# Kernel tuning notes

Hardware: AMD Instinct MI355X
Metric: run time of the kernel (lower is better)

The kernel has to match this reference:

```python
import jax, jax.numpy as jnp
import numpy as np

N_CELLS, D_IN, D_HID, D_OUT, MLP_W = 16384, 512, 1024, 512, 128
N_FACTIONS, SYNC, DEBATE = 8, 0.15, 0.15


def setup_inputs() -> dict:
    key = jax.random.key(0)
    ks = jax.random.split(key, 20)
    s = 0.05
    inp = {
        "x": jax.random.normal(ks[0], (1, D_IN), jnp.float32),
        "hiddens": jax.random.normal(ks[1], (N_CELLS, D_HID), jnp.float32) * 0.1,
        "wealth_norm": jax.random.uniform(ks[2], (N_CELLS,), jnp.float32, 0.5, 1.5),
        "Wa1": jax.random.normal(ks[3], (D_IN + D_HID, MLP_W), jnp.float32) * s,
        "ba1": jax.random.normal(ks[4], (MLP_W,), jnp.float32) * s,
        "Wa2": jax.random.normal(ks[5], (MLP_W, D_OUT), jnp.float32) * s,
        "ba2": jax.random.normal(ks[6], (D_OUT,), jnp.float32) * s,
        "Wg1": jax.random.normal(ks[7], (D_IN + D_HID, MLP_W), jnp.float32) * s,
        "bg1": jax.random.normal(ks[8], (MLP_W,), jnp.float32) * s,
        "Wg2": jax.random.normal(ks[9], (MLP_W, D_OUT), jnp.float32) * s,
        "bg2": jax.random.normal(ks[10], (D_OUT,), jnp.float32) * s,
        "W_ih": jax.random.normal(ks[11], (D_OUT + 1, 3 * D_HID), jnp.float32) * s,
        "W_hh": jax.random.normal(ks[12], (D_HID, 3 * D_HID), jnp.float32) * s,
        "b_ih": jax.random.normal(ks[13], (3 * D_HID,), jnp.float32) * s,
        "b_hh": jax.random.normal(ks[14], (3 * D_HID,), jnp.float32) * s,
        "Wo": jax.random.normal(ks[15], (D_OUT, D_IN), jnp.float32) * s,
        "bo": jax.random.normal(ks[16], (D_IN,), jnp.float32) * s,
        "positions": jax.random.randint(ks[17], (N_CELLS,), 0, 3, jnp.int32) - 1,
        "step": 10,
    }
    return inp


def _gru_cell(mem, h, W_ih, W_hh, b_ih, b_hh):
    # torch.nn.GRUCell math, gate order r, z, n
    gi = mem @ W_ih + b_ih            # [N, 3H]
    gh = h @ W_hh + b_hh              # [N, 3H]
    gi_r, gi_z, gi_n = jnp.split(gi, 3, axis=-1)
    gh_r, gh_z, gh_n = jnp.split(gh, 3, axis=-1)
    r = jax.nn.sigmoid(gi_r + gh_r)
    z = jax.nn.sigmoid(gi_z + gh_z)
    n = jnp.tanh(gi_n + r * gh_n)
    return (1.0 - z) * n + z * h


def _group_sync(h, mask):
    cnt = jnp.sum(mask)
    m = mask[:, None].astype(h.dtype)
    mean = jnp.sum(h * m, axis=0) / jnp.maximum(cnt, 1).astype(h.dtype)
    blended = 0.9 * h + 0.1 * mean
    return jnp.where((mask[:, None]) & (cnt >= 2), blended, h)


def _faction_sync_debate(h, step):
    n = h.shape[0]
    n_f = min(N_FACTIONS, n // 2)
    if n_f < 2:
        return h
    fs = n // n_f
    hf = h[: n_f * fs].reshape(n_f, fs, -1)
    fmean = hf.mean(axis=1, keepdims=True)                    # [n_f, 1, H]
    hf = (1.0 - SYNC) * hf + SYNC * fmean
    if step > 5:
        global_op = hf.mean(axis=1).mean(axis=0)              # [H]
        dc = max(1, fs // 4)
        head = (1.0 - DEBATE) * hf[:, :dc] + DEBATE * global_op
        hf = jnp.concatenate([head, hf[:, dc:]], axis=1)
    out = hf.reshape(n_f * fs, -1)
    if n_f * fs < n:
        out = jnp.concatenate([out, h[n_f * fs:]], axis=0)
    return out


def reference(x, hiddens, wealth_norm, Wa1, ba1, Wa2, ba2, Wg1, bg1, Wg2, bg2,
              W_ih, W_hh, b_ih, b_hh, Wo, bo, positions, step):
    n = hiddens.shape[0]
    xb = jnp.broadcast_to(x, (n, x.shape[-1]))                # same x for every cell
    combined = jnp.concatenate([xb, hiddens], axis=-1)        # [N, D_in+D_hid]
    a = jax.nn.relu(combined @ Wa1 + ba1) @ Wa2 + ba2
    g = jax.nn.relu(combined @ Wg1 + bg1) @ Wg2 + bg2
    output = a - g                                            # [N, D_out]
    tension = jnp.mean(output ** 2, axis=-1, keepdims=True)   # [N, 1]
    mem_input = jax.lax.stop_gradient(jnp.concatenate([output, tension], axis=-1))
    new_h = _gru_cell(mem_input, hiddens, W_ih, W_hh, b_ih, b_hh)
    mod = 0.9 + 0.1 * jnp.clip(wealth_norm, 0.1, 2.0)
    new_h = jnp.clip(new_h * mod[:, None], -10.0, 10.0)
    new_h = jax.lax.stop_gradient(new_h)                      # original detaches state
    new_h = _group_sync(new_h, positions > 0)
    new_h = _group_sync(new_h, positions < 0)
    new_h = _faction_sync_debate(new_h, step)
    # tension weights come from .item() in torch -> constants
    weights = jax.nn.softmax(jax.lax.stop_gradient(tension[:, 0]))
    combined_out = weights @ output                           # [D_out]
    pred = (combined_out @ Wo + bo)[None, :]                  # [1, D_in]
    avg_tension = jnp.mean(tension)
    return pred, avg_tension, new_h
```

## Files before the change

### kernel.cpp

```cpp
#include <hip/hip_runtime.h>
#include <stdint.h>

typedef unsigned short u16;
typedef __bf16 bf16x8 __attribute__((ext_vector_type(8)));
typedef float f32x4 __attribute__((ext_vector_type(4)));


__device__ __forceinline__ float bf2f(unsigned u) { return __uint_as_float(u << 16); }
__device__ __forceinline__ u16 f2bf(float f) {
  unsigned x = __float_as_uint(f);
  unsigned r = x + 0x7fffu + ((x >> 16) & 1u);
  return (u16)(r >> 16);
}
__device__ __forceinline__ void unpack8(uint4 v, float* o) {
  o[0] = bf2f(v.x & 0xffff); o[1] = bf2f(v.x >> 16);
  o[2] = bf2f(v.y & 0xffff); o[3] = bf2f(v.y >> 16);
  o[4] = bf2f(v.z & 0xffff); o[5] = bf2f(v.z >> 16);
  o[6] = bf2f(v.w & 0xffff); o[7] = bf2f(v.w >> 16);
}
__device__ __forceinline__ float sigm(float x) { return 1.f / (1.f + __expf(-x)); }

#define AS1(p) ((const __attribute__((address_space(1))) void*)(p))
#define AS3(p) ((__attribute__((address_space(3))) void*)(p))

#define NC 16384

__global__ void cvt_hid_kernel(const float4* __restrict__ src, uint4* __restrict__ dst) {
  int i = blockIdx.x * 256 + threadIdx.x;
  float4 a = src[(size_t)i * 2], b = src[(size_t)i * 2 + 1];
  union { u16 o[8]; uint4 v; } u;
  u.o[0] = f2bf(a.x); u.o[1] = f2bf(a.y); u.o[2] = f2bf(a.z); u.o[3] = f2bf(a.w);
  u.o[4] = f2bf(b.x); u.o[5] = f2bf(b.y); u.o[6] = f2bf(b.z); u.o[7] = f2bf(b.w);
  dst[i] = u.v;
}

__global__ __launch_bounds__(256) void packT_kernel(
    const float* __restrict__ src, int sld, int srow0,
    u16* __restrict__ dst, int dld, int drow0, int koff,
    int remapThresh, int remapAdd, float sgn) {
  __shared__ float tile[64][65];
  const int k0 = blockIdx.y * 64, c0 = blockIdx.x * 64;
  const int t = threadIdx.x;
  const int tx = t & 15, ty = t >> 4;
#pragma unroll
  for (int p = 0; p < 4; ++p) {
    int r = ty + p * 16;
    float4 v = *reinterpret_cast<const float4*>(&src[(size_t)(srow0 + k0 + r) * sld + c0 + tx * 4]);
    tile[tx * 4 + 0][r] = v.x;
    tile[tx * 4 + 1][r] = v.y;
    tile[tx * 4 + 2][r] = v.z;
    tile[tx * 4 + 3][r] = v.w;
  }
  __syncthreads();
  const int cl = t >> 2;
  const int kb = (t & 3) * 16;
  int col = c0 + cl;
  int row = drow0 + col + ((col >= remapThresh) ? remapAdd : 0);
  union { u16 o[16]; uint4 v[2]; } u;
#pragma unroll
  for (int e = 0; e < 16; ++e) u.o[e] = f2bf(sgn * tile[cl][kb + e]);
  uint4* d = reinterpret_cast<uint4*>(&dst[(size_t)row * dld + koff + k0 + kb]);
  d[0] = u.v[0]; d[1] = u.v[1];
}

__global__ void bias1_kernel(const float* __restrict__ x, const float* __restrict__ Wa1f,
                             const float* __restrict__ ba1f, const float* __restrict__ Wg1f,
                             const float* __restrict__ bg1f, float* __restrict__ bias1) {
  int c = threadIdx.x;
  const float* W = (c < 128) ? Wa1f : Wg1f;
  int cc = c & 127;
  float acc = 0.f;
  int k0 = blockIdx.x * 64;
  for (int k = k0; k < k0 + 64; ++k) acc += x[k] * W[(size_t)k * 128 + cc];
  if (blockIdx.x == 0) acc += (c < 128) ? ba1f[cc] : bg1f[cc];
  atomicAdd(&bias1[c], acc);
}
__global__ void bias2_kernel(const float* __restrict__ ba2f, const float* __restrict__ bg2f,
                             float* __restrict__ bias2) {
  int n = blockIdx.x * 256 + threadIdx.x;
  bias2[n] = ba2f[n] - bg2f[n];
}

__global__ __launch_bounds__(256) void gemm_bt(
    const u16* __restrict__ A0, int lda0, int kbound,
    const u16* __restrict__ A1, int lda1,
    const u16* __restrict__ Bt, int ldb,
    u16* __restrict__ C, int ldc,
    const float* __restrict__ bias, int epi, int Ktot, int gru) {
  __shared__ __align__(16) u16 As[128 * 32];
  __shared__ __align__(16) u16 Bs[128 * 32];
  const int tid = threadIdx.x;
  const int m0 = blockIdx.x * 128;
  const int n0 = blockIdx.y * 128;
  int kbeg = 0, kend = Ktot;
  if (gru) {
    int region = n0 >> 10;
    if (region == 2) kend = 512;
    if (region == 3) kbeg = 512;
  }
  f32x4 acc[4][4] = {};
  const int lane = tid & 63;
  const int w = tid >> 6;
  const int mw = (w & 1) * 64, nw = (w >> 1) * 64;
  const int fr = lane & 15;
  const int kq = (lane >> 4) * 8;
  const int c0 = tid, c1 = tid + 256;
  const int ar0 = c0 >> 2, ak0 = (c0 & 3) * 8;
  const int ar1 = c1 >> 2, ak1 = (c1 & 3) * 8;

  for (int kk = kbeg; kk < kend; kk += 32) {
    const u16* Aseg; int lda, ko;
    if (kk < kbound) { Aseg = A0; lda = lda0; ko = kk; }
    else             { Aseg = A1; lda = lda1; ko = kk - kbound; }
    __syncthreads();
    __builtin_amdgcn_global_load_lds(AS1(Aseg + (size_t)(m0 + ar0) * lda + ko + ak0), AS3(&As[c0 * 8]), 16, 0, 0);
    __builtin_amdgcn_global_load_lds(AS1(Aseg + (size_t)(m0 + ar1) * lda + ko + ak1), AS3(&As[c1 * 8]), 16, 0, 0);
    __builtin_amdgcn_global_load_lds(AS1(Bt + (size_t)(n0 + ar0) * ldb + kk + ak0), AS3(&Bs[c0 * 8]), 16, 0, 0);
    __builtin_amdgcn_global_load_lds(AS1(Bt + (size_t)(n0 + ar1) * ldb + kk + ak1), AS3(&Bs[c1 * 8]), 16, 0, 0);
    __syncthreads();
    bf16x8 af[4], bfv[4];
#pragma unroll
    for (int mt = 0; mt < 4; ++mt)
      af[mt] = *reinterpret_cast<const bf16x8*>(&As[(mw + mt * 16 + fr) * 32 + kq]);
#pragma unroll
    for (int nt = 0; nt < 4; ++nt)
      bfv[nt] = *reinterpret_cast<const bf16x8*>(&Bs[(nw + nt * 16 + fr) * 32 + kq]);
#pragma unroll
    for (int mt = 0; mt < 4; ++mt)
#pragma unroll
      for (int nt = 0; nt < 4; ++nt)
        acc[mt][nt] = __builtin_amdgcn_mfma_f32_16x16x32_bf16(af[mt], bfv[nt], acc[mt][nt], 0, 0, 0);
  }
  const int rq = (lane >> 4) * 4;
#pragma unroll
  for (int mt = 0; mt < 4; ++mt) {
#pragma unroll
    for (int nt = 0; nt < 4; ++nt) {
      int col = n0 + nw + nt * 16 + (lane & 15);
      f32x4 v = acc[mt][nt];
#pragma unroll
      for (int r = 0; r < 4; ++r) {
        int row = m0 + mw + mt * 16 + rq + r;
        float val = v[r];
        if (epi == 1) { val += bias[col]; val = val > 0.f ? val : 0.f; }
        else if (epi == 2) { val += bias[col]; }
        C[(size_t)row * ldc + col] = f2bf(val);
      }
    }
  }
}

__global__ void tension_kernel(const u16* __restrict__ outbf, float* __restrict__ tension) {
  int w = threadIdx.x >> 6, lane = threadIdx.x & 63;
  int row = blockIdx.x * 4 + w;
  uint4 v = *reinterpret_cast<const uint4*>(outbf + (size_t)row * 512 + lane * 8);
  float o[8]; unpack8(v, o);
  float s = 0.f;
#pragma unroll
  for (int e = 0; e < 8; ++e) s += o[e] * o[e];
  for (int off = 32; off; off >>= 1) s += __shfl_down(s, off, 64);
  if (lane == 0) tension[row] = s * (1.f / 512.f);
}

__global__ void gate_kernel(const u16* __restrict__ pre, const u16* __restrict__ hidc,
                            const float* __restrict__ W_ihf, const float* __restrict__ bihf,
                            const float* __restrict__ bhhf, const float* __restrict__ wealthf,
                            const float* __restrict__ tension, u16* __restrict__ hpre,
                            int rowStart) {
  int rl = blockIdx.x, row = rowStart + rl, t = threadIdx.x, j = t * 8;
  const u16* prow = pre + (size_t)rl * 4096;
  const float* wihtf = W_ihf + (size_t)512 * 3072;
  float tv = tension[row];
  float wl = fminf(fmaxf(wealthf[row], 0.1f), 2.0f);
  float mod = 0.9f + 0.1f * wl;
  float pr[8], pz[8], pn1[8], pn2[8], hv[8];
  float wtr[8], wtz[8], wtn[8], bir[8], biz[8], bin_[8], bhn[8], bhr4[8], bhz4[8];
  unpack8(*reinterpret_cast<const uint4*>(prow + j), pr);
  unpack8(*reinterpret_cast<const uint4*>(prow + 1024 + j), pz);
  unpack8(*reinterpret_cast<const uint4*>(prow + 2048 + j), pn1);
  unpack8(*reinterpret_cast<const uint4*>(prow + 3072 + j), pn2);
  unpack8(*reinterpret_cast<const uint4*>(hidc + (size_t)row * 1024 + j), hv);
#pragma unroll
  for (int q = 0; q < 2; ++q) {
    *reinterpret_cast<float4*>(&wtr[q * 4]) = *reinterpret_cast<const float4*>(wihtf + j + q * 4);
    *reinterpret_cast<float4*>(&wtz[q * 4]) = *reinterpret_cast<const float4*>(wihtf + 1024 + j + q * 4);
    *reinterpret_cast<float4*>(&wtn[q * 4]) = *reinterpret_cast<const float4*>(wihtf + 2048 + j + q * 4);
    *reinterpret_cast<float4*>(&bir[q * 4]) = *reinterpret_cast<const float4*>(bihf + j + q * 4);
    *reinterpret_cast<float4*>(&biz[q * 4]) = *reinterpret_cast<const float4*>(bihf + 1024 + j + q * 4);
    *reinterpret_cast<float4*>(&bin_[q * 4]) = *reinterpret_cast<const float4*>(bihf + 2048 + j + q * 4);
    *reinterpret_cast<float4*>(&bhr4[q * 4]) = *reinterpret_cast<const float4*>(bhhf + j + q * 4);
    *reinterpret_cast<float4*>(&bhz4[q * 4]) = *reinterpret_cast<const float4*>(bhhf + 1024 + j + q * 4);
    *reinterpret_cast<float4*>(&bhn[q * 4]) = *reinterpret_cast<const float4*>(bhhf + 2048 + j + q * 4);
  }
  union { u16 o[8]; uint4 v; } u;
#pragma unroll
  for (int e = 0; e < 8; ++e) {
    float r = sigm(pr[e] + tv * wtr[e] + bir[e] + bhr4[e]);
    float z = sigm(pz[e] + tv * wtz[e] + biz[e] + bhz4[e]);
    float n = tanhf(pn1[e] + tv * wtn[e] + bin_[e] + r * (pn2[e] + bhn[e]));
    float h2 = (1.f - z) * n + z * hv[e];
    h2 = fminf(fmaxf(h2 * mod, -10.f), 10.f);
    u.o[e] = f2bf(h2);
  }
  *reinterpret_cast<uint4*>(hpre + (size_t)row * 1024 + j) = u.v;
}

__global__ void count_kernel(const int* __restrict__ positions, int* __restrict__ counts) {
  int i = blockIdx.x * 256 + threadIdx.x;
  if (i < NC) {
    int p = positions[i], f = i >> 11;
    if (p > 0) atomicAdd(&counts[f * 2], 1);
    else if (p < 0) atomicAdd(&counts[f * 2 + 1], 1);
  }
}

__global__ void stats_kernel(const u16* __restrict__ hpre, const int* __restrict__ positions,
                             float* __restrict__ fsums) {
  int cc = blockIdx.x, f = blockIdx.y, z = blockIdx.z, t = threadIdx.x;
  int col = cc * 128 + (t & 127);
  int half = t >> 7;
  float st = 0, sp = 0, sm = 0;
  for (int it = 0; it < 128; ++it) {
    int row = (f << 11) + ((z * 128 + it) << 1) + half;
    int p = positions[row];
    float v = bf2f(hpre[(size_t)row * 1024 + col]);
    st += v;
    if (p > 0) sp += v;
    if (p < 0) sm += v;
  }
  atomicAdd(&fsums[(f * 3 + 0) * 1024 + col], st);
  atomicAdd(&fsums[(f * 3 + 1) * 1024 + col], sp);
  atomicAdd(&fsums[(f * 3 + 2) * 1024 + col], sm);
}

__global__ void derive_kernel(const float* __restrict__ fsums, const int* __restrict__ counts,
                              float* __restrict__ mean1, float* __restrict__ mean2,
                              float* __restrict__ fmean, float* __restrict__ gop,
                              float* __restrict__ scal) {
  int c = threadIdx.x;
  int cnt1 = 0, cnt2 = 0, cf1[8], cf2[8];
#pragma unroll
  for (int f = 0; f < 8; ++f) {
    cf1[f] = counts[f * 2]; cf2[f] = counts[f * 2 + 1];
    cnt1 += cf1[f]; cnt2 += cf2[f];
  }
  float s1 = 0, s2 = 0;
#pragma unroll
  for (int f = 0; f < 8; ++f) { s1 += fsums[(f * 3 + 1) * 1024 + c]; s2 += fsums[(f * 3 + 2) * 1024 + c]; }
  float m1 = s1 / (float)(cnt1 > 1 ? cnt1 : 1);
  float m2 = s2 / (float)(cnt2 > 1 ? cnt2 : 1);
  float a1 = (cnt1 >= 2) ? 0.1f : 0.f;
  float a2 = (cnt2 >= 2) ? 0.1f : 0.f;
  float g = 0;
#pragma unroll
  for (int f = 0; f < 8; ++f) {
    float fm = (fsums[(f * 3) * 1024 + c]
                + a1 * ((float)cf1[f] * m1 - fsums[(f * 3 + 1) * 1024 + c])
                + a2 * ((float)cf2[f] * m2 - fsums[(f * 3 + 2) * 1024 + c])) * (1.f / 2048.f);
    fmean[f * 1024 + c] = fm;
    g += fm;
  }
  gop[c] = g * 0.125f;
  mean1[c] = m1; mean2[c] = m2;
  if (c == 0) { scal[0] = a1; scal[1] = a2; }
}

__global__ void finalize_kernel(const u16* __restrict__ hpre, const int* __restrict__ positions,
                                const int* __restrict__ step, const float* __restrict__ mean1,
                                const float* __restrict__ mean2, const float* __restrict__ fmean,
                                const float* __restrict__ gop, const float* __restrict__ scal,
                                float* __restrict__ out) {
  int row = blockIdx.x, t = threadIdx.x;
  int p = positions[row];
  float w1 = (p > 0) ? scal[0] : 0.f;
  float w2 = (p < 0) ? scal[1] : 0.f;
  int f = row >> 11, q = row & 2047;
  bool deb = (step[0] > 5) && (q < 512);
  const u16* hrow = hpre + (size_t)row * 1024;
  const float* fmp = fmean + f * 1024;
  float* orow = out + 513 + (size_t)row * 1024;
#pragma unroll
  for (int e = 0; e < 8; ++e) {
    int c = e * 128 + t;
    float h = bf2f(hrow[c]);
    float hgs = h + w1 * (mean1[c] - h) + w2 * (mean2[c] - h);
    float hfs = 0.85f * hgs + 0.15f * fmp[c];
    orow[c] = deb ? (0.85f * hfs + 0.15f * gop[c]) : hfs;
  }
}

__global__ void softmax_kernel(const float* __restrict__ tension, float* __restrict__ weights,
                               float* __restrict__ out) {
  __shared__ float red[1024];
  int t = threadIdx.x;
  float tv[16], mx = -1e30f, sumt = 0.f;
#pragma unroll
  for (int k = 0; k < 16; ++k) {
    tv[k] = tension[t + k * 1024];
    mx = fmaxf(mx, tv[k]); sumt += tv[k];
  }
  red[t] = mx; __syncthreads();
  for (int s = 512; s > 0; s >>= 1) { if (t < s) red[t] = fmaxf(red[t], red[t + s]); __syncthreads(); }
  float m = red[0]; __syncthreads();
  red[t] = sumt; __syncthreads();
  for (int s = 512; s > 0; s >>= 1) { if (t < s) red[t] += red[t + s]; __syncthreads(); }
  float tot = red[0]; __syncthreads();
  float ev[16], se = 0.f;
#pragma unroll
  for (int k = 0; k < 16; ++k) { ev[k] = __expf(tv[k] - m); se += ev[k]; }
  red[t] = se; __syncthreads();
  for (int s = 512; s > 0; s >>= 1) { if (t < s) red[t] += red[t + s]; __syncthreads(); }
  float invS = 1.f / red[0];
#pragma unroll
  for (int k = 0; k < 16; ++k) weights[t + k * 1024] = ev[k] * invS;
  if (t == 0) out[512] = tot * (1.f / 16384.f);
}

__global__ void wsum_kernel(const float* __restrict__ weights, const u16* __restrict__ outbf,
                            float* __restrict__ co) {
  int b = blockIdx.x, t = threadIdx.x;
  int c = t * 2;
  float a0 = 0.f, a1 = 0.f;
  int i0 = b * 128;
  for (int i = i0; i < i0 + 128; ++i) {
    float w = weights[i];
    unsigned v = *reinterpret_cast<const unsigned*>(outbf + (size_t)i * 512 + c);
    a0 += w * bf2f(v & 0xffff);
    a1 += w * bf2f(v >> 16);
  }
  atomicAdd(&co[c], a0);
  atomicAdd(&co[c + 1], a1);
}

__global__ void pred_kernel(const float* __restrict__ co, const float* __restrict__ Wof,
                            const float* __restrict__ bof, float* __restrict__ out) {
  __shared__ float cs[512];
  int t = threadIdx.x, n = blockIdx.x * 256 + t;
  cs[t] = co[t]; cs[t + 256] = co[t + 256];
  __syncthreads();
  float acc = bof[n];
  for (int ck = 0; ck < 512; ++ck) acc += cs[ck] * Wof[(size_t)ck * 512 + n];
  out[n] = acc;
}

extern "C" void kernel_launch(void* const* d_in, const int* in_sizes, int n_in,
                              void* d_out, int out_size, void* d_ws, size_t ws_size,
                              hipStream_t stream) {
  const float* x      = (const float*)d_in[0];
  const float* hid    = (const float*)d_in[1];
  const float* wealth = (const float*)d_in[2];
  const float* Wa1    = (const float*)d_in[3];
  const float* ba1    = (const float*)d_in[4];
  const float* Wa2    = (const float*)d_in[5];
  const float* ba2    = (const float*)d_in[6];
  const float* Wg1    = (const float*)d_in[7];
  const float* bg1    = (const float*)d_in[8];
  const float* Wg2    = (const float*)d_in[9];
  const float* bg2    = (const float*)d_in[10];
  const float* W_ih   = (const float*)d_in[11];
  const float* W_hh   = (const float*)d_in[12];
  const float* b_ih   = (const float*)d_in[13];
  const float* b_hh   = (const float*)d_in[14];
  const float* Wo     = (const float*)d_in[15];
  const float* bo     = (const float*)d_in[16];
  const int* positions= (const int*)d_in[17];
  const int* step     = (const int*)d_in[18];
  float* out = (float*)d_out;

  char* w = (char*)d_ws;
  size_t off = 0;
  auto alloc = [&](size_t bytes) { void* p = w + off; off += (bytes + 255) & ~(size_t)255; return p; };
  u16*   hidc    = (u16*)  alloc((size_t)NC * 1024 * 2);
  u16*   outbf   = (u16*)  alloc((size_t)NC * 512 * 2);
  u16*   hpre    = (u16*)  alloc((size_t)NC * 1024 * 2);
  u16*   WgruT   = (u16*)  alloc((size_t)4096 * 1536 * 2);
  u16*   W1catT  = (u16*)  alloc((size_t)256 * 1024 * 2);
  u16*   W2catT  = (u16*)  alloc((size_t)512 * 256 * 2);
  float* bias1   = (float*)alloc(256 * 4);
  float* co      = (float*)alloc(512 * 4);
  int*   counts  = (int*)  alloc(16 * 4);
  float* fsums   = (float*)alloc(8 * 3 * 1024 * 4);
  float* bias2   = (float*)alloc(512 * 4);
  float* tension = (float*)alloc(NC * 4);
  float* weights = (float*)alloc(NC * 4);
  float* mean1   = (float*)alloc(1024 * 4);
  float* mean2   = (float*)alloc(1024 * 4);
  float* gop     = (float*)alloc(1024 * 4);
  float* fmean   = (float*)alloc(8 * 1024 * 4);
  float* scal    = (float*)alloc(8 * 4);
  size_t fixed = off;
  size_t t1Bytes = (size_t)NC * 256 * 2;
  size_t avail = ws_size > fixed ? ws_size - fixed : 0;
  int R = 16384;
  while (R > 1024 && (size_t)R * 4096 * 2 > avail) R >>= 1;
  size_t uBytes = (size_t)R * 4096 * 2; if (uBytes < t1Bytes) uBytes = t1Bytes;
  u16* t1 = (u16*)alloc(uBytes);
  u16* preact = t1;
  int nch = NC / R;

  hipMemsetAsync(bias1, 0, 1024 + 2048 + 256 + 98304, stream);

  cvt_hid_kernel<<<8192, 256, 0, stream>>>((const float4*)hid, (uint4*)hidc);
  packT_kernel<<<dim3(2, 16), 256, 0, stream>>>(Wa1, 128, 512, W1catT, 1024, 0, 0, 1 << 30, 0, 1.f);
  packT_kernel<<<dim3(2, 16), 256, 0, stream>>>(Wg1, 128, 512, W1catT, 1024, 128, 0, 1 << 30, 0, 1.f);
  packT_kernel<<<dim3(8, 2), 256, 0, stream>>>(Wa2, 512, 0, W2catT, 256, 0, 0, 1 << 30, 0, 1.f);
  packT_kernel<<<dim3(8, 2), 256, 0, stream>>>(Wg2, 512, 0, W2catT, 256, 0, 128, 1 << 30, 0, -1.f);
  packT_kernel<<<dim3(48, 8), 256, 0, stream>>>(W_ih, 3072, 0, WgruT, 1536, 0, 0, 1 << 30, 0, 1.f);
  packT_kernel<<<dim3(48, 16), 256, 0, stream>>>(W_hh, 3072, 0, WgruT, 1536, 0, 512, 2048, 1024, 1.f);
  bias1_kernel<<<8, 256, 0, stream>>>(x, Wa1, ba1, Wg1, bg1, bias1);
  bias2_kernel<<<2, 256, 0, stream>>>(ba2, bg2, bias2);
  count_kernel<<<64, 256, 0, stream>>>(positions, counts);

  gemm_bt<<<dim3(128, 2), 256, 0, stream>>>(hidc, 1024, 1024, hidc, 1024,
                                            W1catT, 1024, t1, 256, bias1, 1, 1024, 0);
  gemm_bt<<<dim3(128, 4), 256, 0, stream>>>(t1, 256, 256, t1, 256,
                                            W2catT, 256, outbf, 512, bias2, 2, 256, 0);
  tension_kernel<<<4096, 256, 0, stream>>>(outbf, tension);

  for (int c = 0; c < nch; ++c) {
    const u16* A0 = outbf + (size_t)c * R * 512;
    const u16* A1 = hidc + (size_t)c * R * 1024;
    gemm_bt<<<dim3(R / 128, 32), 256, 0, stream>>>(A0, 512, 512, A1, 1024,
                                                   WgruT, 1536, preact, 4096, nullptr, 0, 1536, 1);
    gate_kernel<<<R, 128, 0, stream>>>(preact, hidc, W_ih, b_ih, b_hh, wealth,
                                       tension, hpre, c * R);
  }

  stats_kernel<<<dim3(8, 8, 8), 256, 0, stream>>>(hpre, positions, fsums);
  derive_kernel<<<1, 1024, 0, stream>>>(fsums, counts, mean1, mean2, fmean, gop, scal);
  finalize_kernel<<<NC, 128, 0, stream>>>(hpre, positions, step, mean1, mean2, fmean, gop,
                                          scal, out);

  softmax_kernel<<<1, 1024, 0, stream>>>(tension, weights, out);
  wsum_kernel<<<128, 256, 0, stream>>>(weights, outbf, co);
  pred_kernel<<<2, 256, 0, stream>>>(co, Wo, bo, out);

  (void)in_sizes; (void)n_in; (void)out_size;
}
```

Measured before the change: 685.3 us.

## Fuse GRU gate math into GEMM epilogue and merge prep/small kernels

Replaces the GRU preactivation GEMM plus a separate gate kernel with one gemm_gru kernel. Each block computes the r, z, n_input and n_hidden tiles for a 64-column slice and applies the gate nonlinearity in registers, so the 16384x4096 bf16 preactivation buffer is never written to or read back from global memory. The tension reduction is folded into the second MLP GEMM's epilogue through shuffles and atomics. The conversion, packing and small bias/count kernels are merged into two launches. The risks are atomic float accumulation order, a fast tanh approximation, and the register pressure of four accumulator sets per block.

```diff
diff --git a/kernel.cpp b/kernel.cpp
--- a/kernel.cpp
+++ b/kernel.cpp
@@ -12,35 +12,23 @@
   unsigned r = x + 0x7fffu + ((x >> 16) & 1u);
   return (u16)(r >> 16);
 }
-__device__ __forceinline__ void unpack8(uint4 v, float* o) {
-  o[0] = bf2f(v.x & 0xffff); o[1] = bf2f(v.x >> 16);
-  o[2] = bf2f(v.y & 0xffff); o[3] = bf2f(v.y >> 16);
-  o[4] = bf2f(v.z & 0xffff); o[5] = bf2f(v.z >> 16);
-  o[6] = bf2f(v.w & 0xffff); o[7] = bf2f(v.w >> 16);
-}
 __device__ __forceinline__ float sigm(float x) { return 1.f / (1.f + __expf(-x)); }
+__device__ __forceinline__ float fast_tanh(float x) {
+  float e = __expf(2.f * x);
+  return 1.f - 2.f / (e + 1.f);
+}
 
 #define AS1(p) ((const __attribute__((address_space(1))) void*)(p))
 #define AS3(p) ((__attribute__((address_space(3))) void*)(p))
 
 #define NC 16384
 
-__global__ void cvt_hid_kernel(const float4* __restrict__ src, uint4* __restrict__ dst) {
-  int i = blockIdx.x * 256 + threadIdx.x;
-  float4 a = src[(size_t)i * 2], b = src[(size_t)i * 2 + 1];
-  union { u16 o[8]; uint4 v; } u;
-  u.o[0] = f2bf(a.x); u.o[1] = f2bf(a.y); u.o[2] = f2bf(a.z); u.o[3] = f2bf(a.w);
-  u.o[4] = f2bf(b.x); u.o[5] = f2bf(b.y); u.o[6] = f2bf(b.z); u.o[7] = f2bf(b.w);
-  dst[i] = u.v;
-}
-
-__global__ __launch_bounds__(256) void packT_kernel(
+__device__ __forceinline__ void packT_body(
     const float* __restrict__ src, int sld, int srow0,
     u16* __restrict__ dst, int dld, int drow0, int koff,
-    int remapThresh, int remapAdd, float sgn) {
-  __shared__ float tile[64][65];
-  const int k0 = blockIdx.y * 64, c0 = blockIdx.x * 64;
-  const int t = threadIdx.x;
+    int remapThresh, int remapAdd, float sgn, int bx, int by,
+    float (*tile)[65], int t) {
+  const int k0 = by * 64, c0 = bx * 64;
   const int tx = t & 15, ty = t >> 4;
 #pragma unroll
   for (int p = 0; p < 4; ++p) {
@@ -63,60 +51,104 @@
   d[0] = u.v[0]; d[1] = u.v[1];
 }
 
-__global__ void bias1_kernel(const float* __restrict__ x, const float* __restrict__ Wa1f,
-                             const float* __restrict__ ba1f, const float* __restrict__ Wg1f,
-                             const float* __restrict__ bg1f, float* __restrict__ bias1) {
-  int c = threadIdx.x;
-  const float* W = (c < 128) ? Wa1f : Wg1f;
-  int cc = c & 127;
-  float acc = 0.f;
-  int k0 = blockIdx.x * 64;
-  for (int k = k0; k < k0 + 64; ++k) acc += x[k] * W[(size_t)k * 128 + cc];
-  if (blockIdx.x == 0) acc += (c < 128) ? ba1f[cc] : bg1f[cc];
-  atomicAdd(&bias1[c], acc);
-}
-__global__ void bias2_kernel(const float* __restrict__ ba2f, const float* __restrict__ bg2f,
-                             float* __restrict__ bias2) {
-  int n = blockIdx.x * 256 + threadIdx.x;
-  bias2[n] = ba2f[n] - bg2f[n];
+__global__ __launch_bounds__(256) void prep_kernel(
+    const float* __restrict__ hid, u16* __restrict__ hidc,
+    const float* __restrict__ W_ih, const float* __restrict__ W_hh, u16* __restrict__ WgruT,
+    const float* __restrict__ Wa1, const float* __restrict__ Wg1, u16* __restrict__ W1catT,
+    const float* __restrict__ Wa2, const float* __restrict__ Wg2, u16* __restrict__ W2catT) {
+  __shared__ float tile[64][65];
+  int b = blockIdx.x, t = threadIdx.x;
+  if (b < 8192) {
+    int i = b * 256 + t;
+    const float4* s = (const float4*)hid;
+    float4 a = s[(size_t)i * 2], c = s[(size_t)i * 2 + 1];
+    union { u16 o[8]; uint4 v; } u;
+    u.o[0] = f2bf(a.x); u.o[1] = f2bf(a.y); u.o[2] = f2bf(a.z); u.o[3] = f2bf(a.w);
+    u.o[4] = f2bf(c.x); u.o[5] = f2bf(c.y); u.o[6] = f2bf(c.z); u.o[7] = f2bf(c.w);
+    ((uint4*)hidc)[i] = u.v;
+    return;
+  }
+  b -= 8192;
+  if (b < 768) {
+    packT_body(W_hh, 3072, 0, WgruT, 1536, 0, 512, 2048, 1024, 1.f, b % 48, b / 48, tile, t);
+    return;
+  }
+  b -= 768;
+  if (b < 384) {
+    packT_body(W_ih, 3072, 0, WgruT, 1536, 0, 0, 1 << 30, 0, 1.f, b % 48, b / 48, tile, t);
+    return;
+  }
+  b -= 384;
+  if (b < 32) {
+    packT_body(Wa1, 128, 512, W1catT, 1024, 0, 0, 1 << 30, 0, 1.f, b % 2, b / 2, tile, t);
+    return;
+  }
+  b -= 32;
+  if (b < 32) {
+    packT_body(Wg1, 128, 512, W1catT, 1024, 128, 0, 1 << 30, 0, 1.f, b % 2, b / 2, tile, t);
+    return;
+  }
+  b -= 32;
+  if (b < 16) {
+    packT_body(Wa2, 512, 0, W2catT, 256, 0, 0, 1 << 30, 0, 1.f, b % 8, b / 8, tile, t);
+    return;
+  }
+  b -= 16;
+  packT_body(Wg2, 512, 0, W2catT, 256, 0, 128, 1 << 30, 0, -1.f, b % 8, b / 8, tile, t);
+}
+
+__global__ void smalls_kernel(const float* __restrict__ x, const float* __restrict__ Wa1,
+                              const float* __restrict__ ba1, const float* __restrict__ Wg1,
+                              const float* __restrict__ bg1, float* __restrict__ bias1,
+                              const float* __restrict__ ba2, const float* __restrict__ bg2,
+                              float* __restrict__ bias2, const int* __restrict__ positions,
+                              int* __restrict__ counts) {
+  int b = blockIdx.x, t = threadIdx.x;
+  if (b < 8) {
+    const float* W = (t < 128) ? Wa1 : Wg1;
+    int cc = t & 127;
+    float acc = 0.f;
+    int k0 = b * 64;
+    for (int k = k0; k < k0 + 64; ++k) acc += x[k] * W[(size_t)k * 128 + cc];
+    if (b == 0) acc += (t < 128) ? ba1[cc] : bg1[cc];
+    atomicAdd(&bias1[t], acc);
+  } else if (b < 10) {
+    int n = (b - 8) * 256 + t;
+    bias2[n] = ba2[n] - bg2[n];
+  } else {
+    int i = (b - 10) * 256 + t;
+    int p = positions[i], f = i >> 11;
+    if (p > 0) atomicAdd(&counts[f * 2], 1);
+    else if (p < 0) atomicAdd(&counts[f * 2 + 1], 1);
+  }
 }
 
 __global__ __launch_bounds__(256) void gemm_bt(
-    const u16* __restrict__ A0, int lda0, int kbound,
-    const u16* __restrict__ A1, int lda1,
+    const u16* __restrict__ A, int lda,
     const u16* __restrict__ Bt, int ldb,
     u16* __restrict__ C, int ldc,
-    const float* __restrict__ bias, int epi, int Ktot, int gru) {
+    const float* __restrict__ bias, int epi, int K,
+    float* __restrict__ tension) {
   __shared__ __align__(16) u16 As[128 * 32];
   __shared__ __align__(16) u16 Bs[128 * 32];
   const int tid = threadIdx.x;
   const int m0 = blockIdx.x * 128;
   const int n0 = blockIdx.y * 128;
-  int kbeg = 0, kend = Ktot;
-  if (gru) {
-    int region = n0 >> 10;
-    if (region == 2) kend = 512;
-    if (region == 3) kbeg = 512;
-  }
   f32x4 acc[4][4] = {};
   const int lane = tid & 63;
   const int w = tid >> 6;
   const int mw = (w & 1) * 64, nw = (w >> 1) * 64;
   const int fr = lane & 15;
   const int kq = (lane >> 4) * 8;
-  const int c0 = tid, c1 = tid + 256;
-  const int ar0 = c0 >> 2, ak0 = (c0 & 3) * 8;
-  const int ar1 = c1 >> 2, ak1 = (c1 & 3) * 8;
-
-  for (int kk = kbeg; kk < kend; kk += 32) {
-    const u16* Aseg; int lda, ko;
-    if (kk < kbound) { Aseg = A0; lda = lda0; ko = kk; }
-    else             { Aseg = A1; lda = lda1; ko = kk - kbound; }
+  const int ar0 = tid >> 2, ak0 = (tid & 3) * 8;
+  const int ar1 = ar0 + 64;
+
+  for (int kk = 0; kk < K; kk += 32) {
     __syncthreads();
-    __builtin_amdgcn_global_load_lds(AS1(Aseg + (size_t)(m0 + ar0) * lda + ko + ak0), AS3(&As[c0 * 8]), 16, 0, 0);
-    __builtin_amdgcn_global_load_lds(AS1(Aseg + (size_t)(m0 + ar1) * lda + ko + ak1), AS3(&As[c1 * 8]), 16, 0, 0);
-    __builtin_amdgcn_global_load_lds(AS1(Bt + (size_t)(n0 + ar0) * ldb + kk + ak0), AS3(&Bs[c0 * 8]), 16, 0, 0);
-    __builtin_amdgcn_global_load_lds(AS1(Bt + (size_t)(n0 + ar1) * ldb + kk + ak1), AS3(&Bs[c1 * 8]), 16, 0, 0);
+    __builtin_amdgcn_global_load_lds(AS1(A + (size_t)(m0 + ar0) * lda + kk + ak0), AS3(&As[tid * 8]), 16, 0, 0);
+    __builtin_amdgcn_global_load_lds(AS1(A + (size_t)(m0 + ar1) * lda + kk + ak0), AS3(&As[(tid + 256) * 8]), 16, 0, 0);
+    __builtin_amdgcn_global_load_lds(AS1(Bt + (size_t)(n0 + ar0) * ldb + kk + ak0), AS3(&Bs[tid * 8]), 16, 0, 0);
+    __builtin_amdgcn_global_load_lds(AS1(Bt + (size_t)(n0 + ar1) * ldb + kk + ak0), AS3(&Bs[(tid + 256) * 8]), 16, 0, 0);
     __syncthreads();
     bf16x8 af[4], bfv[4];
 #pragma unroll
@@ -134,83 +166,130 @@
   const int rq = (lane >> 4) * 4;
 #pragma unroll
   for (int mt = 0; mt < 4; ++mt) {
+    float srow[4] = {0.f, 0.f, 0.f, 0.f};
 #pragma unroll
     for (int nt = 0; nt < 4; ++nt) {
-      int col = n0 + nw + nt * 16 + (lane & 15);
+      int col = n0 + nw + nt * 16 + fr;
       f32x4 v = acc[mt][nt];
 #pragma unroll
       for (int r = 0; r < 4; ++r) {
         int row = m0 + mw + mt * 16 + rq + r;
-        float val = v[r];
-        if (epi == 1) { val += bias[col]; val = val > 0.f ? val : 0.f; }
-        else if (epi == 2) { val += bias[col]; }
+        float val = v[r] + bias[col];
+        if (epi == 1) val = val > 0.f ? val : 0.f;
+        else srow[r] += val * val;
         C[(size_t)row * ldc + col] = f2bf(val);
       }
     }
-  }
-}
-
-__global__ void tension_kernel(const u16* __restrict__ outbf, float* __restrict__ tension) {
-  int w = threadIdx.x >> 6, lane = threadIdx.x & 63;
-  int row = blockIdx.x * 4 + w;
-  uint4 v = *reinterpret_cast<const uint4*>(outbf + (size_t)row * 512 + lane * 8);
-  float o[8]; unpack8(v, o);
-  float s = 0.f;
-#pragma unroll
-  for (int e = 0; e < 8; ++e) s += o[e] * o[e];
-  for (int off = 32; off; off >>= 1) s += __shfl_down(s, off, 64);
-  if (lane == 0) tension[row] = s * (1.f / 512.f);
-}
-
-__global__ void gate_kernel(const u16* __restrict__ pre, const u16* __restrict__ hidc,
-                            const float* __restrict__ W_ihf, const float* __restrict__ bihf,
-                            const float* __restrict__ bhhf, const float* __restrict__ wealthf,
-                            const float* __restrict__ tension, u16* __restrict__ hpre,
-                            int rowStart) {
-  int rl = blockIdx.x, row = rowStart + rl, t = threadIdx.x, j = t * 8;
-  const u16* prow = pre + (size_t)rl * 4096;
-  const float* wihtf = W_ihf + (size_t)512 * 3072;
-  float tv = tension[row];
-  float wl = fminf(fmaxf(wealthf[row], 0.1f), 2.0f);
-  float mod = 0.9f + 0.1f * wl;
-  float pr[8], pz[8], pn1[8], pn2[8], hv[8];
-  float wtr[8], wtz[8], wtn[8], bir[8], biz[8], bin_[8], bhn[8], bhr4[8], bhz4[8];
-  unpack8(*reinterpret_cast<const uint4*>(prow + j), pr);
-  unpack8(*reinterpret_cast<const uint4*>(prow + 1024 + j), pz);
-  unpack8(*reinterpret_cast<const uint4*>(prow + 2048 + j), pn1);
-  unpack8(*reinterpret_cast<const uint4*>(prow + 3072 + j), pn2);
-  unpack8(*reinterpret_cast<const uint4*>(hidc + (size_t)row * 1024 + j), hv);
-#pragma unroll
-  for (int q = 0; q < 2; ++q) {
-    *reinterpret_cast<float4*>(&wtr[q * 4]) = *reinterpret_cast<const float4*>(wihtf + j + q * 4);
-    *reinterpret_cast<float4*>(&wtz[q * 4]) = *reinterpret_cast<const float4*>(wihtf + 1024 + j + q * 4);
-    *reinterpret_cast<float4*>(&wtn[q * 4]) = *reinterpret_cast<const float4*>(wihtf + 2048 + j + q * 4);
-    *reinterpret_cast<float4*>(&bir[q * 4]) = *reinterpret_cast<const float4*>(bihf + j + q * 4);
-    *reinterpret_cast<float4*>(&biz[q * 4]) = *reinterpret_cast<const float4*>(bihf + 1024 + j + q * 4);
-    *reinterpret_cast<float4*>(&bin_[q * 4]) = *reinterpret_cast<const float4*>(bihf + 2048 + j + q * 4);
-    *reinterpret_cast<float4*>(&bhr4[q * 4]) = *reinterpret_cast<const float4*>(bhhf + j + q * 4);
-    *reinterpret_cast<float4*>(&bhz4[q * 4]) = *reinterpret_cast<const float4*>(bhhf + 1024 + j + q * 4);
-    *reinterpret_cast<float4*>(&bhn[q * 4]) = *reinterpret_cast<const float4*>(bhhf + 2048 + j + q * 4);
-  }
-  union { u16 o[8]; uint4 v; } u;
-#pragma unroll
-  for (int e = 0; e < 8; ++e) {
-    float r = sigm(pr[e] + tv * wtr[e] + bir[e] + bhr4[e]);
-    float z = sigm(pz[e] + tv * wtz[e] + biz[e] + bhz4[e]);
-    float n = tanhf(pn1[e] + tv * wtn[e] + bin_[e] + r * (pn2[e] + bhn[e]));
-    float h2 = (1.f - z) * n + z * hv[e];
-    h2 = fminf(fmaxf(h2 * mod, -10.f), 10.f);
-    u.o[e] = f2bf(h2);
-  }
-  *reinterpret_cast<uint4*>(hpre + (size_t)row * 1024 + j) = u.v;
-}
-
-__global__ void count_kernel(const int* __restrict__ positions, int* __restrict__ counts) {
-  int i = blockIdx.x * 256 + threadIdx.x;
-  if (i < NC) {
-    int p = positions[i], f = i >> 11;
-    if (p > 0) atomicAdd(&counts[f * 2], 1);
-    else if (p < 0) atomicAdd(&counts[f * 2 + 1], 1);
+    if (epi == 3) {
+#pragma unroll
+      for (int r = 0; r < 4; ++r) {
+        float s = srow[r];
+        s += __shfl_xor(s, 1, 16); s += __shfl_xor(s, 2, 16);
+        s += __shfl_xor(s, 4, 16); s += __shfl_xor(s, 8, 16);
+        if (fr == 0) atomicAdd(&tension[m0 + mw + mt * 16 + rq + r], s);
+      }
+    }
+  }
+}
+
+__global__ __launch_bounds__(256, 2) void gemm_gru(
+    const u16* __restrict__ outbf, const u16* __restrict__ hidc,
+    const u16* __restrict__ WgruT,
+    const float* __restrict__ W_ihf, const float* __restrict__ bihf,
+    const float* __restrict__ bhhf, const float* __restrict__ wealthf,
+    const float* __restrict__ tension, u16* __restrict__ hpre) {
+  __shared__ __align__(16) u16 As[128 * 32];
+  __shared__ __align__(16) u16 Bs[3][64 * 32];
+  const int tid = threadIdx.x;
+  const int m0 = blockIdx.x * 128;
+  const int j0 = blockIdx.y * 64;
+  f32x4 acc[4][4][2] = {};
+  const int lane = tid & 63;
+  const int w = tid >> 6;
+  const int mw = (w & 1) * 64, nw = (w >> 1) * 32;
+  const int fr = lane & 15;
+  const int kq = (lane >> 4) * 8;
+  const int ar0 = tid >> 2, ak0 = (tid & 3) * 8;
+  const int ar1 = ar0 + 64;
+
+  auto kstep = [&](const u16* Ap, int lda, int ka, int growBase, int gi) {
+    __syncthreads();
+    __builtin_amdgcn_global_load_lds(AS1(Ap + (size_t)(m0 + ar0) * lda + ka + ak0), AS3(&As[tid * 8]), 16, 0, 0);
+    __builtin_amdgcn_global_load_lds(AS1(Ap + (size_t)(m0 + ar1) * lda + ka + ak0), AS3(&As[(tid + 256) * 8]), 16, 0, 0);
+    (void)growBase; (void)gi;
+  };
+  (void)kstep;
+
+#pragma unroll 1
+  for (int phase = 0; phase < 2; ++phase) {
+    const u16* Ap = phase ? hidc : outbf;
+    const int lda = phase ? 1024 : 512;
+    const int kbeg = phase ? 512 : 0;
+    const int kend = phase ? 1536 : 512;
+    const int growG = phase ? 3072 : 2048;
+#pragma unroll 1
+    for (int kk = kbeg; kk < kend; kk += 32) {
+      __syncthreads();
+      int ka = kk - kbeg;
+      __builtin_amdgcn_global_load_lds(AS1(Ap + (size_t)(m0 + ar0) * lda + ka + ak0), AS3(&As[tid * 8]), 16, 0, 0);
+      __builtin_amdgcn_global_load_lds(AS1(Ap + (size_t)(m0 + ar1) * lda + ka + ak0), AS3(&As[(tid + 256) * 8]), 16, 0, 0);
+      __builtin_amdgcn_global_load_lds(AS1(WgruT + (size_t)(j0 + ar0) * 1536 + kk + ak0), AS3(&Bs[0][tid * 8]), 16, 0, 0);
+      __builtin_amdgcn_global_load_lds(AS1(WgruT + (size_t)(1024 + j0 + ar0) * 1536 + kk + ak0), AS3(&Bs[1][tid * 8]), 16, 0, 0);
+      __builtin_amdgcn_global_load_lds(AS1(WgruT + (size_t)(growG + j0 + ar0) * 1536 + kk + ak0), AS3(&Bs[2][tid * 8]), 16, 0, 0);
+      __syncthreads();
+      bf16x8 af[4], b0[2], b1[2], b2[2];
+#pragma unroll
+      for (int mt = 0; mt < 4; ++mt)
+        af[mt] = *reinterpret_cast<const bf16x8*>(&As[(mw + mt * 16 + fr) * 32 + kq]);
+#pragma unroll
+      for (int nt = 0; nt < 2; ++nt) {
+        b0[nt] = *reinterpret_cast<const bf16x8*>(&Bs[0][(nw + nt * 16 + fr) * 32 + kq]);
+        b1[nt] = *reinterpret_cast<const bf16x8*>(&Bs[1][(nw + nt * 16 + fr) * 32 + kq]);
+        b2[nt] = *reinterpret_cast<const bf16x8*>(&Bs[2][(nw + nt * 16 + fr) * 32 + kq]);
+      }
+      int greg = phase ? 3 : 2;
+#pragma unroll
+      for (int mt = 0; mt < 4; ++mt)
+#pragma unroll
+        for (int nt = 0; nt < 2; ++nt) {
+          acc[0][mt][nt] = __builtin_amdgcn_mfma_f32_16x16x32_bf16(af[mt], b0[nt], acc[0][mt][nt], 0, 0, 0);
+          acc[1][mt][nt] = __builtin_amdgcn_mfma_f32_16x16x32_bf16(af[mt], b1[nt], acc[1][mt][nt], 0, 0, 0);
+          acc[greg][mt][nt] = __builtin_amdgcn_mfma_f32_16x16x32_bf16(af[mt], b2[nt], acc[greg][mt][nt], 0, 0, 0);
+        }
+    }
+  }
+
+  const int rq = (lane >> 4) * 4;
+  const float* wt = W_ihf + (size_t)512 * 3072;
+  float wtr[2], wtz[2], wtn[2], bir[2], biz[2], bin_[2], bhr_[2], bhz_[2], bhn_[2];
+#pragma unroll
+  for (int nt = 0; nt < 2; ++nt) {
+    int j = j0 + nw + nt * 16 + fr;
+    wtr[nt] = wt[j]; wtz[nt] = wt[1024 + j]; wtn[nt] = wt[2048 + j];
+    bir[nt] = bihf[j]; biz[nt] = bihf[1024 + j]; bin_[nt] = bihf[2048 + j];
+    bhr_[nt] = bhhf[j]; bhz_[nt] = bhhf[1024 + j]; bhn_[nt] = bhhf[2048 + j];
+  }
+#pragma unroll
+  for (int mt = 0; mt < 4; ++mt) {
+#pragma unroll
+    for (int rr = 0; rr < 4; ++rr) {
+      int row = m0 + mw + mt * 16 + rq + rr;
+      float tv = tension[row] * (1.f / 512.f);
+      float wl = fminf(fmaxf(wealthf[row], 0.1f), 2.0f);
+      float mod = 0.9f + 0.1f * wl;
+#pragma unroll
+      for (int nt = 0; nt < 2; ++nt) {
+        int j = j0 + nw + nt * 16 + fr;
+        float r = sigm(acc[0][mt][nt][rr] + tv * wtr[nt] + bir[nt] + bhr_[nt]);
+        float z = sigm(acc[1][mt][nt][rr] + tv * wtz[nt] + biz[nt] + bhz_[nt]);
+        float n = fast_tanh(acc[2][mt][nt][rr] + tv * wtn[nt] + bin_[nt]
+                            + r * (acc[3][mt][nt][rr] + bhn_[nt]));
+        float h = bf2f(hidc[(size_t)row * 1024 + j]);
+        float h2 = (1.f - z) * n + z * h;
+        h2 = fminf(fmaxf(h2 * mod, -10.f), 10.f);
+        hpre[(size_t)row * 1024 + j] = f2bf(h2);
+      }
+    }
   }
 }
 
@@ -296,7 +375,7 @@
   float tv[16], mx = -1e30f, sumt = 0.f;
 #pragma unroll
   for (int k = 0; k < 16; ++k) {
-    tv[k] = tension[t + k * 1024];
+    tv[k] = tension[t + k * 1024] * (1.f / 512.f);
     mx = fmaxf(mx, tv[k]); sumt += tv[k];
   }
   red[t] = mx; __syncthreads();
@@ -376,55 +455,34 @@
   u16*   WgruT   = (u16*)  alloc((size_t)4096 * 1536 * 2);
   u16*   W1catT  = (u16*)  alloc((size_t)256 * 1024 * 2);
   u16*   W2catT  = (u16*)  alloc((size_t)512 * 256 * 2);
+  u16*   t1      = (u16*)  alloc((size_t)NC * 256 * 2);
   float* bias1   = (float*)alloc(256 * 4);
   float* co      = (float*)alloc(512 * 4);
   int*   counts  = (int*)  alloc(16 * 4);
   float* fsums   = (float*)alloc(8 * 3 * 1024 * 4);
+  float* tension = (float*)alloc(NC * 4);
   float* bias2   = (float*)alloc(512 * 4);
-  float* tension = (float*)alloc(NC * 4);
   float* weights = (float*)alloc(NC * 4);
   float* mean1   = (float*)alloc(1024 * 4);
   float* mean2   = (float*)alloc(1024 * 4);
   float* gop     = (float*)alloc(1024 * 4);
   float* fmean   = (float*)alloc(8 * 1024 * 4);
   float* scal    = (float*)alloc(8 * 4);
-  size_t fixed = off;
-  size_t t1Bytes = (size_t)NC * 256 * 2;
-  size_t avail = ws_size > fixed ? ws_size - fixed : 0;
-  int R = 16384;
-  while (R > 1024 && (size_t)R * 4096 * 2 > avail) R >>= 1;
-  size_t uBytes = (size_t)R * 4096 * 2; if (uBytes < t1Bytes) uBytes = t1Bytes;
-  u16* t1 = (u16*)alloc(uBytes);
-  u16* preact = t1;
-  int nch = NC / R;
-
-  hipMemsetAsync(bias1, 0, 1024 + 2048 + 256 + 98304, stream);
-
-  cvt_hid_kernel<<<8192, 256, 0, stream>>>((const float4*)hid, (uint4*)hidc);
-  packT_kernel<<<dim3(2, 16), 256, 0, stream>>>(Wa1, 128, 512, W1catT, 1024, 0, 0, 1 << 30, 0, 1.f);
-  packT_kernel<<<dim3(2, 16), 256, 0, stream>>>(Wg1, 128, 512, W1catT, 1024, 128, 0, 1 << 30, 0, 1.f);
-  packT_kernel<<<dim3(8, 2), 256, 0, stream>>>(Wa2, 512, 0, W2catT, 256, 0, 0, 1 << 30, 0, 1.f);
-  packT_kernel<<<dim3(8, 2), 256, 0, stream>>>(Wg2, 512, 0, W2catT, 256, 0, 128, 1 << 30, 0, -1.f);
-  packT_kernel<<<dim3(48, 8), 256, 0, stream>>>(W_ih, 3072, 0, WgruT, 1536, 0, 0, 1 << 30, 0, 1.f);
-  packT_kernel<<<dim3(48, 16), 256, 0, stream>>>(W_hh, 3072, 0, WgruT, 1536, 0, 512, 2048, 1024, 1.f);
-  bias1_kernel<<<8, 256, 0, stream>>>(x, Wa1, ba1, Wg1, bg1, bias1);
-  bias2_kernel<<<2, 256, 0, stream>>>(ba2, bg2, bias2);
-  count_kernel<<<64, 256, 0, stream>>>(positions, counts);
-
-  gemm_bt<<<dim3(128, 2), 256, 0, stream>>>(hidc, 1024, 1024, hidc, 1024,
-                                            W1catT, 1024, t1, 256, bias1, 1, 1024, 0);
-  gemm_bt<<<dim3(128, 4), 256, 0, stream>>>(t1, 256, 256, t1, 256,
-                                            W2catT, 256, outbf, 512, bias2, 2, 256, 0);
-  tension_kernel<<<4096, 256, 0, stream>>>(outbf, tension);
-
-  for (int c = 0; c < nch; ++c) {
-    const u16* A0 = outbf + (size_t)c * R * 512;
-    const u16* A1 = hidc + (size_t)c * R * 1024;
-    gemm_bt<<<dim3(R / 128, 32), 256, 0, stream>>>(A0, 512, 512, A1, 1024,
-                                                   WgruT, 1536, preact, 4096, nullptr, 0, 1536, 1);
-    gate_kernel<<<R, 128, 0, stream>>>(preact, hidc, W_ih, b_ih, b_hh, wealth,
-                                       tension, hpre, c * R);
-  }
+
+  hipMemsetAsync(bias1, 0, 1024 + 2048 + 256 + 98304 + 65536, stream);
+
+  prep_kernel<<<9440, 256, 0, stream>>>(hid, hidc, W_ih, W_hh, WgruT,
+                                        Wa1, Wg1, W1catT, Wa2, Wg2, W2catT);
+  smalls_kernel<<<74, 256, 0, stream>>>(x, Wa1, ba1, Wg1, bg1, bias1,
+                                        ba2, bg2, bias2, positions, counts);
+
+  gemm_bt<<<dim3(128, 2), 256, 0, stream>>>(hidc, 1024, W1catT, 1024, t1, 256,
+                                            bias1, 1, 1024, nullptr);
+  gemm_bt<<<dim3(128, 4), 256, 0, stream>>>(t1, 256, W2catT, 256, outbf, 512,
+                                            bias2, 3, 256, tension);
+
+  gemm_gru<<<dim3(128, 16), 256, 0, stream>>>(outbf, hidc, WgruT, W_ih, b_ih, b_hh,
+                                              wealth, tension, hpre);
 
   stats_kernel<<<dim3(8, 8, 8), 256, 0, stream>>>(hpre, positions, fsums);
   derive_kernel<<<1, 1024, 0, stream>>>(fsums, counts, mean1, mean2, fmean, gop, scal);
@@ -435,5 +493,5 @@
   wsum_kernel<<<128, 256, 0, stream>>>(weights, outbf, co);
   pred_kernel<<<2, 256, 0, stream>>>(co, Wo, bo, out);
 
-  (void)in_sizes; (void)n_in; (void)out_size;
-}
+  (void)in_sizes; (void)n_in; (void)out_size; (void)ws_size;
+}
```

After: 630.1 us. 1.09x faster.
